# Kernel tuning notes

Hardware: AMD Instinct MI355X
Metric: run time of the kernel (lower is better)

## Reference

```python
import jax, jax.numpy as jnp
import numpy as np

DIM = 256
HEADS = 4
HEAD_DIM = DIM // HEADS          # 64
KEY_DIM = HEAD_DIM // 2          # 32 (attn_ratio=0.5)
HIDDEN = DIM + 2 * KEY_DIM * HEADS  # 512
B, H, W = 2, 64, 64
EPS = 1e-5


def _conv2d(x, w, groups=1, pad=0):
    return jax.lax.conv_general_dilated(
        x, w, window_strides=(1, 1), padding=[(pad, pad), (pad, pad)],
        dimension_numbers=('NCHW', 'OIHW', 'NCHW'), feature_group_count=groups)


def _bn(x, g, b, m, v):
    scale = g / jnp.sqrt(v + EPS)
    return x * scale[None, :, None, None] + (b - m * scale)[None, :, None, None]


def setup_inputs() -> dict:
    key = jax.random.key(0)
    ks = jax.random.split(key, 16)
    d = {
        'x': jax.random.normal(ks[0], (B, DIM, H, W), jnp.float32),
        'qkv_w': jax.random.normal(ks[1], (HIDDEN, DIM, 1, 1), jnp.float32) * 0.05,
        'qkv_g': jax.random.uniform(ks[2], (HIDDEN,), jnp.float32, 0.5, 1.5),
        'qkv_b': jax.random.normal(ks[3], (HIDDEN,), jnp.float32) * 0.1,
        'qkv_m': jax.random.normal(ks[4], (HIDDEN,), jnp.float32) * 0.1,
        'qkv_v': jax.random.uniform(ks[5], (HIDDEN,), jnp.float32, 0.5, 1.5),
        'proj_w': jax.random.normal(ks[6], (DIM, DIM, 1, 1), jnp.float32) * 0.05,
        'proj_g': jax.random.uniform(ks[7], (DIM,), jnp.float32, 0.5, 1.5),
        'proj_b': jax.random.normal(ks[8], (DIM,), jnp.float32) * 0.1,
        'proj_m': jax.random.normal(ks[9], (DIM,), jnp.float32) * 0.1,
        'proj_v': jax.random.uniform(ks[10], (DIM,), jnp.float32, 0.5, 1.5),
        'pe_w': jax.random.normal(ks[11], (DIM, 1, 3, 3), jnp.float32) * 0.1,
        'pe_g': jax.random.uniform(ks[12], (DIM,), jnp.float32, 0.5, 1.5),
        'pe_b': jax.random.normal(ks[13], (DIM,), jnp.float32) * 0.1,
        'pe_m': jax.random.normal(ks[14], (DIM,), jnp.float32) * 0.1,
        'pe_v': jax.random.uniform(ks[15], (DIM,), jnp.float32, 0.5, 1.5),
    }
    return d


def reference(x, qkv_w, qkv_g, qkv_b, qkv_m, qkv_v,
              proj_w, proj_g, proj_b, proj_m, proj_v,
              pe_w, pe_g, pe_b, pe_m, pe_v):
    b, c, h, w = x.shape
    n = h * w
    scale = KEY_DIM ** -0.5

    qkv = _bn(_conv2d(x, qkv_w), qkv_g, qkv_b, qkv_m, qkv_v)  # [b, hidden, h, w]
    qkv = qkv.reshape(b, HEADS, 2 * KEY_DIM + HEAD_DIM, n)
    q = qkv[:, :, :KEY_DIM]                       # [b, heads, key_dim, n]
    k = qkv[:, :, KEY_DIM:2 * KEY_DIM]            # [b, heads, key_dim, n]
    v = qkv[:, :, 2 * KEY_DIM:]                   # [b, heads, head_dim, n]

    # attn[b,h,i,j] = sum_d q[b,h,d,i] * k[b,h,d,j] * scale; softmax over j
    attn = jnp.einsum('bhdi,bhdj->bhij', q, k) * scale
    attn = jax.nn.softmax(attn, axis=-1)

    # y = v @ attn^T : out[b,h,d,i] = sum_j v[b,h,d,j] * attn[b,h,i,j]
    y = jnp.einsum('bhdj,bhij->bhdi', v, attn).reshape(b, c, h, w)

    pe = _bn(_conv2d(v.reshape(b, c, h, w), pe_w, groups=c, pad=1),
             pe_g, pe_b, pe_m, pe_v)
    y = y + pe
    return _bn(_conv2d(y, proj_w), proj_g, proj_b, proj_m, proj_v)
```

## Files before the change

### kernel.cpp

```cpp
#include <hip/hip_runtime.h>
#include <hip/hip_bf16.h>

#define NSP 4096
#define BEPS 1e-5f
#define JSPLIT 4
#define JCHUNK (NSP / JSPLIT)

using short8  = __attribute__((ext_vector_type(8))) short;
using f32x4   = __attribute__((ext_vector_type(4))) float;

#define SCALE_LOG2E 0.25500526940103816f

__device__ __forceinline__ float b2f(unsigned short u) {
  return __uint_as_float(((unsigned)u) << 16);
}
__device__ __forceinline__ unsigned short f2b(float x) {
  unsigned u = __float_as_uint(x);
  u += 0x7fffu + ((u >> 16) & 1u);
  return (unsigned short)(u >> 16);
}
__device__ __forceinline__ unsigned pk_bf16(float a, float b) {
  return ((unsigned)f2b(b) << 16) | (unsigned)f2b(a);
}

__global__ __launch_bounds__(256) void cast_w_kernel(
    const float* __restrict__ qkv_w, const float* __restrict__ proj_w,
    unsigned short* __restrict__ wqb, unsigned short* __restrict__ wpb)
{
  const int i = blockIdx.x * 256 + threadIdx.x;
  if (i < 131072)       wqb[i] = f2b(qkv_w[i]);
  else                  wpb[i - 131072] = f2b(proj_w[i - 131072]);
}

__global__ __launch_bounds__(256) void transpose_x_kernel(
    const float* __restrict__ x, unsigned short* __restrict__ xT)
{
  const int n0 = blockIdx.x * 64, c0 = blockIdx.y * 64, b = blockIdx.z;
  __shared__ __align__(16) unsigned short tx[64][72];
  const int t = threadIdx.x;
  const int row = t >> 2;
  const int seg = t & 3;
  {
    const float* xp = x + ((size_t)(b * 256 + c0 + row)) * NSP + n0 + seg * 16;
    #pragma unroll
    for (int q4 = 0; q4 < 4; ++q4) {
      const float4 a = *reinterpret_cast<const float4*>(xp + q4 * 4);
      tx[seg * 16 + q4 * 4 + 0][row] = f2b(a.x);
      tx[seg * 16 + q4 * 4 + 1][row] = f2b(a.y);
      tx[seg * 16 + q4 * 4 + 2][row] = f2b(a.z);
      tx[seg * 16 + q4 * 4 + 3][row] = f2b(a.w);
    }
  }
  __syncthreads();
  const int nrow = t >> 2, ch = t & 3;
  unsigned short* op = xT + ((size_t)(b * NSP + n0 + nrow)) * 256 + c0 + ch * 16;
  *reinterpret_cast<float4*>(op)     = *reinterpret_cast<const float4*>(&tx[nrow][ch * 16]);
  *reinterpret_cast<float4*>(op + 8) = *reinterpret_cast<const float4*>(&tx[nrow][ch * 16 + 8]);
}

__global__ __launch_bounds__(256) void qkv_gemm_kernel(
    const unsigned short* __restrict__ xT, const unsigned short* __restrict__ wqb,
    const float* __restrict__ gg, const float* __restrict__ bb,
    const float* __restrict__ mm, const float* __restrict__ vv,
    unsigned short* __restrict__ qb, unsigned short* __restrict__ kb,
    unsigned short* __restrict__ vb)
{
  const int n0 = blockIdx.x * 64;
  const int cotile = blockIdx.y;
  const int b = blockIdx.z;
  const int co0 = cotile * 64;
  const int t = threadIdx.x;
  __shared__ __align__(16) unsigned short wt[64][136];
  __shared__ __align__(16) unsigned short xt[64][136];
  const int lane = t & 63, wave = t >> 6;
  const int m16 = lane & 15, quad = lane >> 4;
  const int row = t >> 2, seg = t & 3;

  f32x4 acc[4] = {};
  for (int kc = 0; kc < 2; ++kc) {
    if (kc) __syncthreads();
    {
      const unsigned short* wp = wqb + (size_t)(co0 + row) * 256 + kc * 128 + seg * 32;
      const unsigned short* xp = xT + ((size_t)(b * NSP + n0 + row)) * 256 + kc * 128 + seg * 32;
      #pragma unroll
      for (int u = 0; u < 4; ++u) {
        *reinterpret_cast<float4*>(&wt[row][seg * 32 + u * 8]) =
            *reinterpret_cast<const float4*>(wp + u * 8);
        *reinterpret_cast<float4*>(&xt[row][seg * 32 + u * 8]) =
            *reinterpret_cast<const float4*>(xp + u * 8);
      }
    }
    __syncthreads();
    if ((cotile & 1) == 0) {
      #pragma unroll
      for (int ks = 0; ks < 4; ++ks) {
        const short8 af = *reinterpret_cast<const short8*>(&wt[wave * 16 + m16][ks * 32 + quad * 8]);
        #pragma unroll
        for (int nt = 0; nt < 4; ++nt) {
          const short8 bf = *reinterpret_cast<const short8*>(&xt[nt * 16 + m16][ks * 32 + quad * 8]);
          acc[nt] = __builtin_amdgcn_mfma_f32_16x16x32_bf16(af, bf, acc[nt], 0, 0, 0);
        }
      }
    } else {
      #pragma unroll
      for (int ks = 0; ks < 4; ++ks) {
        const short8 bf = *reinterpret_cast<const short8*>(&wt[wave * 16 + m16][ks * 32 + quad * 8]);
        #pragma unroll
        for (int nt = 0; nt < 4; ++nt) {
          const short8 af = *reinterpret_cast<const short8*>(&xt[nt * 16 + m16][ks * 32 + quad * 8]);
          acc[nt] = __builtin_amdgcn_mfma_f32_16x16x32_bf16(af, bf, acc[nt], 0, 0, 0);
        }
      }
    }
  }

  const int head = cotile >> 1;
  const int bh = b * 4 + head;
  if ((cotile & 1) == 0) {
    const int coh = wave * 16 + quad * 4;
    float sc[4], bi[4];
    #pragma unroll
    for (int r = 0; r < 4; ++r) {
      const int c = co0 + coh + r;
      sc[r] = gg[c] * rsqrtf(vv[c] + BEPS);
      bi[r] = bb[c] - mm[c] * sc[r];
    }
    unsigned short* dst = (coh < 32) ? qb : kb;
    const int d0 = coh & 31;
    #pragma unroll
    for (int nt = 0; nt < 4; ++nt) {
      const int i = n0 + nt * 16 + m16;
      uint2 pk2;
      pk2.x = pk_bf16(acc[nt][0] * sc[0] + bi[0], acc[nt][1] * sc[1] + bi[1]);
      pk2.y = pk_bf16(acc[nt][2] * sc[2] + bi[2], acc[nt][3] * sc[3] + bi[3]);
      *reinterpret_cast<uint2*>(dst + ((size_t)bh * NSP + i) * 32 + d0) = pk2;
    }
  } else {
    const int c = co0 + wave * 16 + m16;
    const float sc = gg[c] * rsqrtf(vv[c] + BEPS);
    const float bi = bb[c] - mm[c] * sc;
    const int d = wave * 16 + m16;
    #pragma unroll
    for (int nt = 0; nt < 4; ++nt) {
      const int j = n0 + nt * 16 + quad * 4;
      uint2 pk2;
      pk2.x = pk_bf16(acc[nt][0] * sc + bi, acc[nt][1] * sc + bi);
      pk2.y = pk_bf16(acc[nt][2] * sc + bi, acc[nt][3] * sc + bi);
      *reinterpret_cast<uint2*>(vb + ((size_t)(bh * 64 + d)) * NSP + j) = pk2;
    }
  }
}

__global__ __launch_bounds__(256, 3) void attn_kernel(
    const unsigned short* __restrict__ qb, const unsigned short* __restrict__ kb,
    const unsigned short* __restrict__ vb,
    unsigned short* __restrict__ Opart, float* __restrict__ lpart)
{
  const int i0    = blockIdx.x * 128;
  const int bh    = blockIdx.y;
  const int split = blockIdx.z;
  const int jbase = split * JCHUNK;
  const int t  = threadIdx.x;
  const int lane = t & 63, wave = t >> 6;
  const int m16 = lane & 15, quad = lane >> 4;
  __shared__ __align__(16) short qs[128][40];
  __shared__ __align__(16) short ks[64][40];
  __shared__ __align__(16) short vs[64][72];
  __shared__ __align__(16) short ps[128][72];

  {
    const unsigned short* qp = qb + ((size_t)bh * NSP + i0) * 32;
    const int r = t >> 1, h = t & 1;
    *reinterpret_cast<float4*>(&qs[r][h * 16]) =
        *reinterpret_cast<const float4*>(qp + r * 32 + h * 16);
    *reinterpret_cast<float4*>(&qs[r][h * 16 + 8]) =
        *reinterpret_cast<const float4*>(qp + r * 32 + h * 16 + 8);
  }
  __syncthreads();
  short8 qfrag[2];
  qfrag[0] = *reinterpret_cast<const short8*>(&qs[wave * 32 + m16][quad * 8]);
  qfrag[1] = *reinterpret_cast<const short8*>(&qs[wave * 32 + 16 + m16][quad * 8]);

  float rsum[2] = {0.f, 0.f};
  f32x4 oacc[2][4] = {};

  const int srow = t >> 2, schunk = t & 3;
  for (int jt0 = 0; jt0 < JCHUNK; jt0 += 64) {
    const int j0 = jbase + jt0;
    __syncthreads();
    {
      const unsigned short* kp = kb + ((size_t)bh * NSP + j0) * 32;
      *reinterpret_cast<float4*>(&ks[srow][schunk * 8]) =
          *reinterpret_cast<const float4*>(kp + srow * 32 + schunk * 8);
      const unsigned short* vp = vb + (size_t)bh * 64 * NSP + j0;
      *reinterpret_cast<float4*>(&vs[srow][schunk * 16]) =
          *reinterpret_cast<const float4*>(vp + (size_t)srow * NSP + schunk * 16);
      *reinterpret_cast<float4*>(&vs[srow][schunk * 16 + 8]) =
          *reinterpret_cast<const float4*>(vp + (size_t)srow * NSP + schunk * 16 + 8);
    }
    __syncthreads();

    short8 kf[4];
    #pragma unroll
    for (int jt = 0; jt < 4; ++jt)
      kf[jt] = *reinterpret_cast<const short8*>(&ks[jt * 16 + m16][quad * 8]);

    #pragma unroll
    for (int it = 0; it < 2; ++it) {
      f32x4 sacc[4];
      #pragma unroll
      for (int jt = 0; jt < 4; ++jt)
        sacc[jt] = __builtin_amdgcn_mfma_f32_16x16x32_bf16(kf[jt], qfrag[it],
                                                           (f32x4){0.f,0.f,0.f,0.f}, 0, 0, 0);
      const int irow = wave * 32 + it * 16 + m16;
      #pragma unroll
      for (int jt = 0; jt < 4; ++jt) {
        float p0 = __builtin_amdgcn_exp2f(sacc[jt][0] * SCALE_LOG2E);
        float p1 = __builtin_amdgcn_exp2f(sacc[jt][1] * SCALE_LOG2E);
        float p2 = __builtin_amdgcn_exp2f(sacc[jt][2] * SCALE_LOG2E);
        float p3 = __builtin_amdgcn_exp2f(sacc[jt][3] * SCALE_LOG2E);
        rsum[it] += (p0 + p1) + (p2 + p3);
        uint2 pk2;
        pk2.x = pk_bf16(p0, p1);
        pk2.y = pk_bf16(p2, p3);
        *reinterpret_cast<uint2*>(&ps[irow][jt * 16 + quad * 4]) = pk2;
      }
    }

    short8 pa[2][2];
    #pragma unroll
    for (int it = 0; it < 2; ++it) {
      pa[it][0] = *reinterpret_cast<const short8*>(&ps[wave * 32 + it * 16 + m16][quad * 8]);
      pa[it][1] = *reinterpret_cast<const short8*>(&ps[wave * 32 + it * 16 + m16][32 + quad * 8]);
    }
    #pragma unroll
    for (int dt = 0; dt < 4; ++dt) {
      const short8 v0 = *reinterpret_cast<const short8*>(&vs[dt * 16 + m16][quad * 8]);
      const short8 v1 = *reinterpret_cast<const short8*>(&vs[dt * 16 + m16][32 + quad * 8]);
      #pragma unroll
      for (int it = 0; it < 2; ++it) {
        oacc[it][dt] = __builtin_amdgcn_mfma_f32_16x16x32_bf16(pa[it][0], v0, oacc[it][dt], 0, 0, 0);
        oacc[it][dt] = __builtin_amdgcn_mfma_f32_16x16x32_bf16(pa[it][1], v1, oacc[it][dt], 0, 0, 0);
      }
    }
  }

  #pragma unroll
  for (int it = 0; it < 2; ++it) {
    float rs = rsum[it];
    rs += __shfl_xor(rs, 16);
    rs += __shfl_xor(rs, 32);
    if (quad == 0)
      lpart[((size_t)split * 8 + bh) * NSP + i0 + wave * 32 + it * 16 + m16] = rs;
  }

  #pragma unroll
  for (int it = 0; it < 2; ++it)
    #pragma unroll
    for (int dt = 0; dt < 4; ++dt) {
      const int d = dt * 16 + m16;
      uint2 pk2;
      pk2.x = pk_bf16(oacc[it][dt][0], oacc[it][dt][1]);
      pk2.y = pk_bf16(oacc[it][dt][2], oacc[it][dt][3]);
      *reinterpret_cast<uint2*>(Opart +
          (((size_t)split * 8 + bh) * 64 + d) * NSP + i0 + wave * 32 + it * 16 + quad * 4) = pk2;
    }
}

__global__ __launch_bounds__(256) void fuse_kernel(
    const unsigned short* __restrict__ Opart, const float* __restrict__ lpart,
    const unsigned short* __restrict__ vb,
    const float* __restrict__ pw, const float* __restrict__ pg,
    const float* __restrict__ pb, const float* __restrict__ pm,
    const float* __restrict__ pv,
    unsigned short* __restrict__ yT)
{
  const int py = blockIdx.x;
  const int bh = blockIdx.y;
  const int b = bh >> 2, h = bh & 3;
  const int t = threadIdx.x;
  const int d = t >> 2, seg = t & 3;
  __shared__ float lsum[64];
  __shared__ __align__(16) unsigned short yt[64][72];

  if (t < 64) {
    float ls = 0.f;
    #pragma unroll
    for (int s = 0; s < JSPLIT; ++s)
      ls += lpart[((size_t)s * 8 + bh) * NSP + py * 64 + t];
    lsum[t] = ls;
  }
  __syncthreads();

  const int c = h * 64 + d;
  const int i0 = py * 64 + seg * 16;
  float os[16] = {};
  #pragma unroll
  for (int s = 0; s < JSPLIT; ++s) {
    const unsigned short* op = Opart + (((size_t)s * 8 + bh) * 64 + d) * NSP + i0;
    #pragma unroll
    for (int u = 0; u < 16; ++u) os[u] += b2f(op[u]);
  }

  float w9[9];
  #pragma unroll
  for (int i = 0; i < 9; ++i) w9[i] = pw[c * 9 + i];
  const float sc = pg[c] * rsqrtf(pv[c] + BEPS);
  const float bi = pb[c] - pm[c] * sc;
  const unsigned short* vrow = vb + ((size_t)(bh * 64 + d)) * NSP;

  float conv[16] = {};
  #pragma unroll
  for (int dy = -1; dy <= 1; ++dy) {
    const int yy = py + dy;
    if (yy < 0 || yy > 63) continue;
    float vals[18];
    #pragma unroll
    for (int u = 0; u < 18; ++u) {
      const int px = seg * 16 - 1 + u;
      vals[u] = (px >= 0 && px < 64) ? b2f(vrow[yy * 64 + px]) : 0.f;
    }
    const float wr0 = w9[(dy + 1) * 3 + 0], wr1 = w9[(dy + 1) * 3 + 1], wr2 = w9[(dy + 1) * 3 + 2];
    #pragma unroll
    for (int u = 0; u < 16; ++u)
      conv[u] += vals[u] * wr0 + vals[u + 1] * wr1 + vals[u + 2] * wr2;
  }

  #pragma unroll
  for (int u = 0; u < 16; ++u) {
    const float yv = os[u] / lsum[seg * 16 + u] + conv[u] * sc + bi;
    yt[seg * 16 + u][d] = f2b(yv);
  }
  __syncthreads();

  const int prow = t >> 2, ch = t & 3;
  unsigned short* op = yT + ((size_t)(b * NSP + py * 64 + prow)) * 256 + h * 64 + ch * 16;
  *reinterpret_cast<float4*>(op)     = *reinterpret_cast<const float4*>(&yt[prow][ch * 16]);
  *reinterpret_cast<float4*>(op + 8) = *reinterpret_cast<const float4*>(&yt[prow][ch * 16 + 8]);
}

__global__ __launch_bounds__(256) void proj_gemm_kernel(
    const unsigned short* __restrict__ yT, const unsigned short* __restrict__ wpb,
    const float* __restrict__ gg, const float* __restrict__ bb,
    const float* __restrict__ mm, const float* __restrict__ vv,
    float* __restrict__ out)
{
  const int n0 = blockIdx.x * 64;
  const int co0 = blockIdx.y * 64;
  const int b = blockIdx.z;
  const int t = threadIdx.x;
  __shared__ __align__(16) unsigned short wt[64][136];
  __shared__ __align__(16) unsigned short yt[64][136];
  const int lane = t & 63, wave = t >> 6;
  const int m16 = lane & 15, quad = lane >> 4;
  const int row = t >> 2, seg = t & 3;

  f32x4 acc[4] = {};
  for (int kc = 0; kc < 2; ++kc) {
    if (kc) __syncthreads();
    {
      const unsigned short* wp = wpb + (size_t)(co0 + row) * 256 + kc * 128 + seg * 32;
      const unsigned short* yp = yT + ((size_t)(b * NSP + n0 + row)) * 256 + kc * 128 + seg * 32;
      #pragma unroll
      for (int u = 0; u < 4; ++u) {
        *reinterpret_cast<float4*>(&wt[row][seg * 32 + u * 8]) =
            *reinterpret_cast<const float4*>(wp + u * 8);
        *reinterpret_cast<float4*>(&yt[row][seg * 32 + u * 8]) =
            *reinterpret_cast<const float4*>(yp + u * 8);
      }
    }
    __syncthreads();
    #pragma unroll
    for (int ks = 0; ks < 4; ++ks) {
      const short8 bf = *reinterpret_cast<const short8*>(&wt[wave * 16 + m16][ks * 32 + quad * 8]);
      #pragma unroll
      for (int nt = 0; nt < 4; ++nt) {
        const short8 af = *reinterpret_cast<const short8*>(&yt[nt * 16 + m16][ks * 32 + quad * 8]);
        acc[nt] = __builtin_amdgcn_mfma_f32_16x16x32_bf16(af, bf, acc[nt], 0, 0, 0);
      }
    }
  }

  const int c = co0 + wave * 16 + m16;
  const float sc = gg[c] * rsqrtf(vv[c] + BEPS);
  const float bi = bb[c] - mm[c] * sc;
  #pragma unroll
  for (int nt = 0; nt < 4; ++nt) {
    const int n = n0 + nt * 16 + quad * 4;
    float4 ov;
    ov.x = acc[nt][0] * sc + bi; ov.y = acc[nt][1] * sc + bi;
    ov.z = acc[nt][2] * sc + bi; ov.w = acc[nt][3] * sc + bi;
    *reinterpret_cast<float4*>(out + ((size_t)(b * 256 + c)) * NSP + n) = ov;
  }
}

extern "C" void kernel_launch(void* const* d_in, const int* in_sizes, int n_in,
                              void* d_out, int out_size, void* d_ws, size_t ws_size,
                              hipStream_t stream)
{
  const float* x      = (const float*)d_in[0];
  const float* qkv_w  = (const float*)d_in[1];
  const float* qkv_g  = (const float*)d_in[2];
  const float* qkv_b  = (const float*)d_in[3];
  const float* qkv_m  = (const float*)d_in[4];
  const float* qkv_v  = (const float*)d_in[5];
  const float* proj_w = (const float*)d_in[6];
  const float* proj_g = (const float*)d_in[7];
  const float* proj_b = (const float*)d_in[8];
  const float* proj_m = (const float*)d_in[9];
  const float* proj_v = (const float*)d_in[10];
  const float* pe_w   = (const float*)d_in[11];
  const float* pe_g   = (const float*)d_in[12];
  const float* pe_b   = (const float*)d_in[13];
  const float* pe_m   = (const float*)d_in[14];
  const float* pe_v   = (const float*)d_in[15];
  float* out = (float*)d_out;

  unsigned short* qb = (unsigned short*)d_ws;
  unsigned short* kb = qb + (size_t)8 * NSP * 32;
  unsigned short* vb = kb + (size_t)8 * NSP * 32;
  unsigned short* Opart = vb + (size_t)8 * 64 * NSP;
  float* lpart = (float*)(Opart + (size_t)JSPLIT * 8 * 64 * NSP);
  unsigned short* xT = (unsigned short*)(lpart + (size_t)JSPLIT * 8 * NSP);
  unsigned short* yT = xT + (size_t)2 * NSP * 256;
  unsigned short* wqb = yT + (size_t)2 * NSP * 256;
  unsigned short* wpb = wqb + (size_t)512 * 256;

  cast_w_kernel<<<dim3(768), 256, 0, stream>>>(qkv_w, proj_w, wqb, wpb);
  transpose_x_kernel<<<dim3(64, 4, 2), 256, 0, stream>>>(x, xT);
  qkv_gemm_kernel<<<dim3(64, 8, 2), 256, 0, stream>>>(xT, wqb, qkv_g, qkv_b, qkv_m, qkv_v,
                                                      qb, kb, vb);
  attn_kernel<<<dim3(32, 8, JSPLIT), 256, 0, stream>>>(qb, kb, vb, Opart, lpart);
  fuse_kernel<<<dim3(64, 8), 256, 0, stream>>>(Opart, lpart, vb,
                                               pe_w, pe_g, pe_b, pe_m, pe_v, yT);
  proj_gemm_kernel<<<dim3(64, 4, 2), 256, 0, stream>>>(yT, wpb, proj_g, proj_b, proj_m, proj_v,
                                                       out);
}
```

Measured before the change: 169.9 us.

## Widen GEMM spatial tiles, alias attention LDS buffers, vectorize fuse loads

```diff
diff --git a/kernel.cpp b/kernel.cpp
--- a/kernel.cpp
+++ b/kernel.cpp
@@ -13,6 +13,12 @@
 
 __device__ __forceinline__ float b2f(unsigned short u) {
   return __uint_as_float(((unsigned)u) << 16);
+}
+__device__ __forceinline__ float b2f_lo(unsigned w) {
+  return __uint_as_float(w << 16);
+}
+__device__ __forceinline__ float b2f_hi(unsigned w) {
+  return __uint_as_float(w & 0xffff0000u);
 }
 __device__ __forceinline__ unsigned short f2b(float x) {
   unsigned u = __float_as_uint(x);
@@ -65,30 +71,30 @@
     unsigned short* __restrict__ qb, unsigned short* __restrict__ kb,
     unsigned short* __restrict__ vb)
 {
-  const int n0 = blockIdx.x * 64;
+  const int n0 = blockIdx.x * 128;
   const int cotile = blockIdx.y;
   const int b = blockIdx.z;
   const int co0 = cotile * 64;
   const int t = threadIdx.x;
   __shared__ __align__(16) unsigned short wt[64][136];
-  __shared__ __align__(16) unsigned short xt[64][136];
+  __shared__ __align__(16) unsigned short xt[128][136];
   const int lane = t & 63, wave = t >> 6;
   const int m16 = lane & 15, quad = lane >> 4;
-  const int row = t >> 2, seg = t & 3;
-
-  f32x4 acc[4] = {};
+
+  f32x4 acc[8] = {};
   for (int kc = 0; kc < 2; ++kc) {
     if (kc) __syncthreads();
     {
-      const unsigned short* wp = wqb + (size_t)(co0 + row) * 256 + kc * 128 + seg * 32;
-      const unsigned short* xp = xT + ((size_t)(b * NSP + n0 + row)) * 256 + kc * 128 + seg * 32;
-      #pragma unroll
-      for (int u = 0; u < 4; ++u) {
-        *reinterpret_cast<float4*>(&wt[row][seg * 32 + u * 8]) =
+      const unsigned short* wp = wqb + (size_t)(co0 + (t >> 2)) * 256 + kc * 128 + (t & 3) * 32;
+      #pragma unroll
+      for (int u = 0; u < 4; ++u)
+        *reinterpret_cast<float4*>(&wt[t >> 2][(t & 3) * 32 + u * 8]) =
             *reinterpret_cast<const float4*>(wp + u * 8);
-        *reinterpret_cast<float4*>(&xt[row][seg * 32 + u * 8]) =
+      const unsigned short* xp = xT + ((size_t)(b * NSP + n0 + (t >> 1))) * 256 + kc * 128 + (t & 1) * 64;
+      #pragma unroll
+      for (int u = 0; u < 8; ++u)
+        *reinterpret_cast<float4*>(&xt[t >> 1][(t & 1) * 64 + u * 8]) =
             *reinterpret_cast<const float4*>(xp + u * 8);
-      }
     }
     __syncthreads();
     if ((cotile & 1) == 0) {
@@ -96,7 +102,7 @@
       for (int ks = 0; ks < 4; ++ks) {
         const short8 af = *reinterpret_cast<const short8*>(&wt[wave * 16 + m16][ks * 32 + quad * 8]);
         #pragma unroll
-        for (int nt = 0; nt < 4; ++nt) {
+        for (int nt = 0; nt < 8; ++nt) {
           const short8 bf = *reinterpret_cast<const short8*>(&xt[nt * 16 + m16][ks * 32 + quad * 8]);
           acc[nt] = __builtin_amdgcn_mfma_f32_16x16x32_bf16(af, bf, acc[nt], 0, 0, 0);
         }
@@ -106,7 +112,7 @@
       for (int ks = 0; ks < 4; ++ks) {
         const short8 bf = *reinterpret_cast<const short8*>(&wt[wave * 16 + m16][ks * 32 + quad * 8]);
         #pragma unroll
-        for (int nt = 0; nt < 4; ++nt) {
+        for (int nt = 0; nt < 8; ++nt) {
           const short8 af = *reinterpret_cast<const short8*>(&xt[nt * 16 + m16][ks * 32 + quad * 8]);
           acc[nt] = __builtin_amdgcn_mfma_f32_16x16x32_bf16(af, bf, acc[nt], 0, 0, 0);
         }
@@ -128,7 +134,7 @@
     unsigned short* dst = (coh < 32) ? qb : kb;
     const int d0 = coh & 31;
     #pragma unroll
-    for (int nt = 0; nt < 4; ++nt) {
+    for (int nt = 0; nt < 8; ++nt) {
       const int i = n0 + nt * 16 + m16;
       uint2 pk2;
       pk2.x = pk_bf16(acc[nt][0] * sc[0] + bi[0], acc[nt][1] * sc[1] + bi[1]);
@@ -141,7 +147,7 @@
     const float bi = bb[c] - mm[c] * sc;
     const int d = wave * 16 + m16;
     #pragma unroll
-    for (int nt = 0; nt < 4; ++nt) {
+    for (int nt = 0; nt < 8; ++nt) {
       const int j = n0 + nt * 16 + quad * 4;
       uint2 pk2;
       pk2.x = pk_bf16(acc[nt][0] * sc + bi, acc[nt][1] * sc + bi);
@@ -151,7 +157,7 @@
   }
 }
 
-__global__ __launch_bounds__(256, 3) void attn_kernel(
+__global__ __launch_bounds__(256, 5) void attn_kernel(
     const unsigned short* __restrict__ qb, const unsigned short* __restrict__ kb,
     const unsigned short* __restrict__ vb,
     unsigned short* __restrict__ Opart, float* __restrict__ lpart)
@@ -163,10 +169,11 @@
   const int t  = threadIdx.x;
   const int lane = t & 63, wave = t >> 6;
   const int m16 = lane & 15, quad = lane >> 4;
-  __shared__ __align__(16) short qs[128][40];
-  __shared__ __align__(16) short ks[64][40];
-  __shared__ __align__(16) short vs[64][72];
-  __shared__ __align__(16) short ps[128][72];
+  __shared__ __align__(16) short smem[16384];
+  short (*qs)[40] = (short(*)[40])smem;
+  short (*ps)[72] = (short(*)[72])smem;
+  short (*ks)[40] = (short(*)[40])(smem + 9216);
+  short (*vs)[72] = (short(*)[72])(smem + 9216 + 2560);
 
   {
     const unsigned short* qp = qb + ((size_t)bh * NSP + i0) * 32;
@@ -297,9 +304,17 @@
   float os[16] = {};
   #pragma unroll
   for (int s = 0; s < JSPLIT; ++s) {
-    const unsigned short* op = Opart + (((size_t)s * 8 + bh) * 64 + d) * NSP + i0;
-    #pragma unroll
-    for (int u = 0; u < 16; ++u) os[u] += b2f(op[u]);
+    const uint4* op = reinterpret_cast<const uint4*>(
+        Opart + (((size_t)s * 8 + bh) * 64 + d) * NSP + i0);
+    const uint4 a = op[0], e = op[1];
+    os[0]  += b2f_lo(a.x); os[1]  += b2f_hi(a.x);
+    os[2]  += b2f_lo(a.y); os[3]  += b2f_hi(a.y);
+    os[4]  += b2f_lo(a.z); os[5]  += b2f_hi(a.z);
+    os[6]  += b2f_lo(a.w); os[7]  += b2f_hi(a.w);
+    os[8]  += b2f_lo(e.x); os[9]  += b2f_hi(e.x);
+    os[10] += b2f_lo(e.y); os[11] += b2f_hi(e.y);
+    os[12] += b2f_lo(e.z); os[13] += b2f_hi(e.z);
+    os[14] += b2f_lo(e.w); os[15] += b2f_hi(e.w);
   }
 
   float w9[9];
@@ -314,12 +329,20 @@
   for (int dy = -1; dy <= 1; ++dy) {
     const int yy = py + dy;
     if (yy < 0 || yy > 63) continue;
+    const unsigned short* vr = vrow + yy * 64 + seg * 16;
     float vals[18];
-    #pragma unroll
-    for (int u = 0; u < 18; ++u) {
-      const int px = seg * 16 - 1 + u;
-      vals[u] = (px >= 0 && px < 64) ? b2f(vrow[yy * 64 + px]) : 0.f;
-    }
+    const uint4 m0 = *reinterpret_cast<const uint4*>(vr);
+    const uint4 m1 = *reinterpret_cast<const uint4*>(vr + 8);
+    vals[1]  = b2f_lo(m0.x); vals[2]  = b2f_hi(m0.x);
+    vals[3]  = b2f_lo(m0.y); vals[4]  = b2f_hi(m0.y);
+    vals[5]  = b2f_lo(m0.z); vals[6]  = b2f_hi(m0.z);
+    vals[7]  = b2f_lo(m0.w); vals[8]  = b2f_hi(m0.w);
+    vals[9]  = b2f_lo(m1.x); vals[10] = b2f_hi(m1.x);
+    vals[11] = b2f_lo(m1.y); vals[12] = b2f_hi(m1.y);
+    vals[13] = b2f_lo(m1.z); vals[14] = b2f_hi(m1.z);
+    vals[15] = b2f_lo(m1.w); vals[16] = b2f_hi(m1.w);
+    vals[0]  = (seg > 0) ? b2f_hi(*reinterpret_cast<const unsigned*>(vr - 2)) : 0.f;
+    vals[17] = (seg < 3) ? b2f_lo(*reinterpret_cast<const unsigned*>(vr + 16)) : 0.f;
     const float wr0 = w9[(dy + 1) * 3 + 0], wr1 = w9[(dy + 1) * 3 + 1], wr2 = w9[(dy + 1) * 3 + 2];
     #pragma unroll
     for (int u = 0; u < 16; ++u)
@@ -345,36 +368,36 @@
     const float* __restrict__ mm, const float* __restrict__ vv,
     float* __restrict__ out)
 {
-  const int n0 = blockIdx.x * 64;
+  const int n0 = blockIdx.x * 128;
   const int co0 = blockIdx.y * 64;
   const int b = blockIdx.z;
   const int t = threadIdx.x;
   __shared__ __align__(16) unsigned short wt[64][136];
-  __shared__ __align__(16) unsigned short yt[64][136];
+  __shared__ __align__(16) unsigned short yt[128][136];
   const int lane = t & 63, wave = t >> 6;
   const int m16 = lane & 15, quad = lane >> 4;
-  const int row = t >> 2, seg = t & 3;
-
-  f32x4 acc[4] = {};
+
+  f32x4 acc[8] = {};
   for (int kc = 0; kc < 2; ++kc) {
     if (kc) __syncthreads();
     {
-      const unsigned short* wp = wpb + (size_t)(co0 + row) * 256 + kc * 128 + seg * 32;
-      const unsigned short* yp = yT + ((size_t)(b * NSP + n0 + row)) * 256 + kc * 128 + seg * 32;
-      #pragma unroll
-      for (int u = 0; u < 4; ++u) {
-        *reinterpret_cast<float4*>(&wt[row][seg * 32 + u * 8]) =
+      const unsigned short* wp = wpb + (size_t)(co0 + (t >> 2)) * 256 + kc * 128 + (t & 3) * 32;
+      #pragma unroll
+      for (int u = 0; u < 4; ++u)
+        *reinterpret_cast<float4*>(&wt[t >> 2][(t & 3) * 32 + u * 8]) =
             *reinterpret_cast<const float4*>(wp + u * 8);
-        *reinterpret_cast<float4*>(&yt[row][seg * 32 + u * 8]) =
+      const unsigned short* yp = yT + ((size_t)(b * NSP + n0 + (t >> 1))) * 256 + kc * 128 + (t & 1) * 64;
+      #pragma unroll
+      for (int u = 0; u < 8; ++u)
+        *reinterpret_cast<float4*>(&yt[t >> 1][(t & 1) * 64 + u * 8]) =
             *reinterpret_cast<const float4*>(yp + u * 8);
-      }
     }
     __syncthreads();
     #pragma unroll
     for (int ks = 0; ks < 4; ++ks) {
       const short8 bf = *reinterpret_cast<const short8*>(&wt[wave * 16 + m16][ks * 32 + quad * 8]);
       #pragma unroll
-      for (int nt = 0; nt < 4; ++nt) {
+      for (int nt = 0; nt < 8; ++nt) {
         const short8 af = *reinterpret_cast<const short8*>(&yt[nt * 16 + m16][ks * 32 + quad * 8]);
         acc[nt] = __builtin_amdgcn_mfma_f32_16x16x32_bf16(af, bf, acc[nt], 0, 0, 0);
       }
@@ -385,7 +408,7 @@
   const float sc = gg[c] * rsqrtf(vv[c] + BEPS);
   const float bi = bb[c] - mm[c] * sc;
   #pragma unroll
-  for (int nt = 0; nt < 4; ++nt) {
+  for (int nt = 0; nt < 8; ++nt) {
     const int n = n0 + nt * 16 + quad * 4;
     float4 ov;
     ov.x = acc[nt][0] * sc + bi; ov.y = acc[nt][1] * sc + bi;
@@ -428,11 +451,11 @@
 
   cast_w_kernel<<<dim3(768), 256, 0, stream>>>(qkv_w, proj_w, wqb, wpb);
   transpose_x_kernel<<<dim3(64, 4, 2), 256, 0, stream>>>(x, xT);
-  qkv_gemm_kernel<<<dim3(64, 8, 2), 256, 0, stream>>>(xT, wqb, qkv_g, qkv_b, qkv_m, qkv_v,
+  qkv_gemm_kernel<<<dim3(32, 8, 2), 256, 0, stream>>>(xT, wqb, qkv_g, qkv_b, qkv_m, qkv_v,
                                                       qb, kb, vb);
   attn_kernel<<<dim3(32, 8, JSPLIT), 256, 0, stream>>>(qb, kb, vb, Opart, lpart);
   fuse_kernel<<<dim3(64, 8), 256, 0, stream>>>(Opart, lpart, vb,
                                                pe_w, pe_g, pe_b, pe_m, pe_v, yT);
-  proj_gemm_kernel<<<dim3(64, 4, 2), 256, 0, stream>>>(yT, wpb, proj_g, proj_b, proj_m, proj_v,
+  proj_gemm_kernel<<<dim3(32, 4, 2), 256, 0, stream>>>(yT, wpb, proj_g, proj_b, proj_m, proj_v,
                                                        out);
 }
```

Result: slower. 188.8 us (+11.1%).
